# Kernel tuning notes

Measured on AMD Instinct MI355X. Metric: run time of the kernel, lower is better.

## Reference

```python
import jax, jax.numpy as jnp
import numpy as np

N_NODES = 50000
N_EDGES = 800000
G_DIM = 128
H1 = 32
HEADS = 4
H2 = 64
ATT_SLOPE = 0.2   # PyG GATConv default negative_slope
LRELU_SLOPE = 0.01  # F.leaky_relu default
BN_EPS = 1e-5


def segment_softmax(logits, seg, num_segments):
    # numerically stable softmax over edges grouped by destination node
    m = jax.ops.segment_max(logits, seg, num_segments=num_segments)
    e = jnp.exp(logits - m[seg])
    s = jax.ops.segment_sum(e, seg, num_segments=num_segments)
    return e / (s[seg] + 1e-16)


def gat_layer(x, src, dst, W, a_src, a_dst, bias, concat):
    # PyG GATConv: x' = W x ; alpha_e = softmax_dst(leaky_relu(a_src.x_src + a_dst.x_dst))
    N = x.shape[0]
    H, C = a_src.shape
    xw = (x @ W).reshape(N, H, C)          # [N,H,C]
    al_s = jnp.sum(xw * a_src, axis=-1)    # [N,H]
    al_d = jnp.sum(xw * a_dst, axis=-1)    # [N,H]
    logits = jax.nn.leaky_relu(al_s[src] + al_d[dst], ATT_SLOPE)  # [E,H]
    alpha = segment_softmax(logits, dst, N)                        # [E,H]
    out = jax.ops.segment_sum(alpha[:, :, None] * xw[src], dst, num_segments=N)  # [N,H,C]
    out = out.reshape(N, H * C) if concat else out.mean(axis=1)
    return out + bias


def batchnorm_train(x, gamma, beta):
    mu = x.mean(axis=0)
    var = x.var(axis=0)  # biased, as torch BN uses for normalization
    return (x - mu) * jax.lax.rsqrt(var + BN_EPS) * gamma + beta


def setup_inputs() -> dict:
    key = jax.random.key(0)
    ks = jax.random.split(key, 12)
    node_features = jax.random.normal(ks[0], (N_NODES, G_DIM), dtype=jnp.float32)
    node_type = jax.random.randint(ks[1], (N_NODES,), 0, 3)
    edge_index = jax.random.randint(ks[2], (2, N_EDGES), 0, N_NODES)
    s1 = 1.0 / np.sqrt(G_DIM)
    s2 = 1.0 / np.sqrt(H1 * HEADS)
    return {
        "node_features": node_features,
        "node_type": node_type,
        "edge_index": edge_index,
        "W1": jax.random.normal(ks[3], (G_DIM, HEADS * H1), dtype=jnp.float32) * s1,
        "a_src1": jax.random.normal(ks[4], (HEADS, H1), dtype=jnp.float32) * s1,
        "a_dst1": jax.random.normal(ks[5], (HEADS, H1), dtype=jnp.float32) * s1,
        "b1": jnp.zeros((HEADS * H1,), dtype=jnp.float32),
        "g1": jnp.ones((HEADS * H1,), dtype=jnp.float32),
        "beta1": jnp.zeros((HEADS * H1,), dtype=jnp.float32),
        "W2": jax.random.normal(ks[6], (HEADS * H1, H2), dtype=jnp.float32) * s2,
        "a_src2": jax.random.normal(ks[7], (1, H2), dtype=jnp.float32) * s2,
        "a_dst2": jax.random.normal(ks[8], (1, H2), dtype=jnp.float32) * s2,
        "b2": jnp.zeros((H2,), dtype=jnp.float32),
        "g2": jnp.ones((H2,), dtype=jnp.float32),
        "beta2": jnp.zeros((H2,), dtype=jnp.float32),
    }


def reference(node_features, node_type, edge_index, W1, a_src1, a_dst1, b1, g1, beta1,
              W2, a_src2, a_dst2, b2, g2, beta2):
    N = node_features.shape[0]
    loop = jnp.arange(N)
    src = jnp.concatenate([edge_index[0], loop])  # add_self_loops=True (PyG default)
    dst = jnp.concatenate([edge_index[1], loop])
    x = gat_layer(node_features, src, dst, W1, a_src1, a_dst1, b1, concat=True)
    x = jax.nn.leaky_relu(batchnorm_train(x, g1, beta1), LRELU_SLOPE)
    x = gat_layer(x, src, dst, W2, a_src2, a_dst2, b2, concat=False)
    x = jax.nn.leaky_relu(batchnorm_train(x, g2, beta2), LRELU_SLOPE)
    return x
```

## Files before the change

kernel.cpp:

```cpp
#include <hip/hip_runtime.h>
#include <hip/hip_fp16.h>

#define NN 50000
#define NE 800000
#define ET 850000
#define GD 128
#define D1 128
#define NH 4
#define D2 64
#define NB_SCAN 196
#define NBP 1024
#define NXCD 8
#define NPX 6250
#define NSB 32
#define ESL 26563
#define NHB 256
#define CAP 8192

typedef unsigned short u16;
typedef _Float16 half8_t __attribute__((ext_vector_type(8)));
typedef float    f32x4_t __attribute__((ext_vector_type(4)));

__device__ __forceinline__ float lrelu(float x, float s) { return x > 0.f ? x : s * x; }

__global__ void k_prepw(const float* __restrict__ W1, const float* __restrict__ W2,
                        __half* __restrict__ Wp1, __half* __restrict__ Wp2) {
    int idx = blockIdx.x * 256 + threadIdx.x;
    if (idx < 16384) {
        int i = idx & 7, l = (idx >> 3) & 63, nt = (idx >> 9) & 7, kk = idx >> 12;
        int k = kk * 32 + (l >> 4) * 8 + i, n = nt * 16 + (l & 15);
        Wp1[idx] = __float2half(W1[k * D1 + n]);
    } else if (idx < 24576) {
        int x2 = idx - 16384;
        int i = x2 & 7, l = (x2 >> 3) & 63, nt = (x2 >> 9) & 3, kk = x2 >> 11;
        int k = kk * 32 + (l >> 4) * 8 + i, n = nt * 16 + (l & 15);
        Wp2[x2] = __float2half(W2[k * D2 + n]);
    }
}

__global__ void k_histgemm1(const int* __restrict__ ei,
                            unsigned* __restrict__ ulist, u16* __restrict__ plist,
                            int* __restrict__ partial, int* __restrict__ mcount,
                            const float* __restrict__ x, const half8_t* __restrict__ wp,
                            const float* __restrict__ as, const float* __restrict__ ad,
                            __half* __restrict__ xw, float* __restrict__ al_s,
                            float* __restrict__ al_d) {
    __shared__ unsigned lh[NPX];
    __shared__ unsigned lk;
    if (blockIdx.x < NHB) {
        const int s = blockIdx.x & (NXCD - 1), j = blockIdx.x >> 3;
        const int lo = s * NPX;
        for (int i = threadIdx.x; i < NPX; i += 256) lh[i] = 0u;
        if (threadIdx.x == 0) lk = 0u;
        __syncthreads();
        const int e0 = j * ESL, e1 = min(ET, e0 + ESL);
        const size_t ub = (size_t)blockIdx.x * CAP;
        for (int e = e0 + threadIdx.x; e < e1; e += 256) {
            int d = (e < NE) ? ei[NE + e] : (e - NE);
            unsigned dl = (unsigned)(d - lo);
            if (dl < (unsigned)NPX) {
                unsigned p = atomicAdd(&lh[dl], 1u);
                int src = (e < NE) ? ei[e] : d;
                unsigned k = atomicAdd(&lk, 1u);
                ulist[ub + k] = (dl << 16) | (unsigned)src;
                plist[ub + k] = (u16)p;
            }
        }
        __syncthreads();
        const size_t pb = ((size_t)s * NSB + j) * NPX;
        for (int i = threadIdx.x; i < NPX; i += 256) partial[pb + i] = (int)lh[i];
        if (threadIdx.x == 0) mcount[blockIdx.x] = (int)lk;
        return;
    }
    const int strip = (blockIdx.x - NHB) * 4 + (threadIdx.x >> 6);
    if (strip >= NN / 16) return;
    const int l = threadIdx.x & 63;
    const int row0 = strip * 16;
    const int c = l & 15, g = l >> 4;
    const float* xrow = x + (size_t)(row0 + c) * GD;

    f32x4_t acc[8];
#pragma unroll
    for (int nt = 0; nt < 8; nt++) acc[nt] = (f32x4_t){0.f, 0.f, 0.f, 0.f};

#pragma unroll
    for (int kk = 0; kk < 4; kk++) {
        const int koff = kk * 32 + g * 8;
        f32x4_t a0 = *(const f32x4_t*)(xrow + koff);
        f32x4_t a1 = *(const f32x4_t*)(xrow + koff + 4);
        half8_t af;
#pragma unroll
        for (int i = 0; i < 4; i++) { af[i] = (_Float16)a0[i]; af[i + 4] = (_Float16)a1[i]; }
#pragma unroll
        for (int nt = 0; nt < 8; nt++) {
            half8_t bf = wp[(kk * 8 + nt) * 64 + l];
            acc[nt] = __builtin_amdgcn_mfma_f32_16x16x32_f16(af, bf, acc[nt], 0, 0, 0);
        }
    }

    float asv[8], adv[8];
#pragma unroll
    for (int nt = 0; nt < 8; nt++) { asv[nt] = as[nt * 16 + c]; adv[nt] = ad[nt * 16 + c]; }

#pragma unroll
    for (int r = 0; r < 4; r++) {
        const int row = row0 + g * 4 + r;
        __half* xwr = xw + (size_t)row * D1;
        float hs[4] = {0.f, 0.f, 0.f, 0.f}, hd[4] = {0.f, 0.f, 0.f, 0.f};
#pragma unroll
        for (int nt = 0; nt < 8; nt++) {
            float v = acc[nt][r];
            xwr[nt * 16 + c] = __float2half(v);
            hs[nt >> 1] += v * asv[nt];
            hd[nt >> 1] += v * adv[nt];
        }
#pragma unroll
        for (int m = 1; m <= 8; m <<= 1) {
#pragma unroll
            for (int h = 0; h < 4; h++) { hs[h] += __shfl_xor(hs[h], m); hd[h] += __shfl_xor(hd[h], m); }
        }
        if (c == 0) {
#pragma unroll
            for (int h = 0; h < 4; h++) { al_s[row * NH + h] = hs[h]; al_d[row * NH + h] = hd[h]; }
        }
    }
}

__global__ void k_nodeprefix(const int* __restrict__ partial, int* __restrict__ P,
                             int* __restrict__ cnt) {
    int d = blockIdx.x * 256 + threadIdx.x;
    if (d >= NN) return;
    int s = d / NPX, dl = d - s * NPX;
    size_t base = (size_t)s * NSB * NPX + dl;
    int run = 0;
    for (int j = 0; j < NSB; j++) {
        size_t idx = base + (size_t)j * NPX;
        P[idx] = run;
        run += partial[idx];
    }
    cnt[d] = run;
}

__global__ void k_blocksum(const int* __restrict__ cnt, int* __restrict__ part) {
    __shared__ int r[256];
    int t = threadIdx.x, i = blockIdx.x * 256 + t;
    r[t] = (i < NN) ? cnt[i] : 0;
    __syncthreads();
    for (int s = 128; s >= 1; s >>= 1) {
        if (t < s) r[t] += r[t + s];
        __syncthreads();
    }
    if (t == 0) part[blockIdx.x] = r[0];
}

__global__ void k_scanfix(const int* __restrict__ cnt, const int* __restrict__ part,
                          int* __restrict__ row_ptr) {
    __shared__ int pp[256];
    __shared__ int r[256];
    int b = blockIdx.x, t = threadIdx.x, i = b * 256 + t;
    pp[t] = (t < NB_SCAN) ? part[t] : 0;
    int v = (i < NN) ? cnt[i] : 0;
    r[t] = v;
    __syncthreads();
    for (int off = 1; off < 256; off <<= 1) {
        int pv = (t >= off) ? pp[t - off] : 0;
        int rv = (t >= off) ? r[t - off] : 0;
        __syncthreads();
        pp[t] += pv; r[t] += rv;
        __syncthreads();
    }
    int pbase = b ? pp[b - 1] : 0;
    if (i < NN) row_ptr[i] = pbase + (t ? r[t - 1] : 0);
    if (i == NN - 1) row_ptr[NN] = pbase + r[t];
}

__global__ void k_fill_x(const int* __restrict__ row_ptr, const int* __restrict__ P,
                         const unsigned* __restrict__ ulist, const u16* __restrict__ plist,
                         const int* __restrict__ mcount, u16* __restrict__ csr_src) {
    const int b = blockIdx.x;
    const int s = b & (NXCD - 1), j = b >> 3;
    const int lo = s * NPX;
    const int m = mcount[b];
    const size_t ub = (size_t)b * CAP;
    const size_t pb = ((size_t)s * NSB + j) * NPX;
    for (int k = threadIdx.x; k < m; k += 256) {
        unsigned u = ulist[ub + k];
        unsigned p = plist[ub + k];
        int dl = (int)(u >> 16);
        int base = row_ptr[lo + dl] + P[pb + dl];
        csr_src[base + p] = (u16)(u & 0xffffu);
    }
}

__global__ void k_gat1(const int* __restrict__ row_ptr, const u16* __restrict__ csr_src,
                       const float* __restrict__ als, const float* __restrict__ ald,
                       const __half2* __restrict__ xw, __half2* __restrict__ out) {
    const int b = blockIdx.x;
    const int d = (b & (NXCD - 1)) * NPX + (b >> 3);
    const int beg = row_ptr[d];
    const int deg = row_ptr[d + 1] - beg;
    const int lane = threadIdx.x;

    __shared__ int   s_src[64];
    __shared__ float s_al[64 * NH];

    const float4 adv = *(const float4*)(ald + d * NH);
    const int h = lane >> 4;

    float ax = 0.f, ay = 0.f, den = 0.f;
    for (int base = 0; base < deg; base += 64) {
        int cnt = min(64, deg - base);
        if (lane < cnt) {
            int s = csr_src[beg + base + lane];
            s_src[lane] = s;
            const float4 a = *(const float4*)(als + s * NH);
            s_al[lane * NH + 0] = __expf(lrelu(a.x + adv.x, 0.2f));
            s_al[lane * NH + 1] = __expf(lrelu(a.y + adv.y, 0.2f));
            s_al[lane * NH + 2] = __expf(lrelu(a.z + adv.z, 0.2f));
            s_al[lane * NH + 3] = __expf(lrelu(a.w + adv.w, 0.2f));
        }
        __syncthreads();
#pragma unroll 4
        for (int i = 0; i < cnt; i++) {
            float al = s_al[i * NH + h];
            float2 v = __half22float2(xw[(size_t)s_src[i] * 64 + lane]);
            den += al; ax += al * v.x; ay += al * v.y;
        }
        __syncthreads();
    }
    float inv = 1.f / (den + 1e-16f);
    __half2 hv;
    hv.x = __float2half(ax * inv);
    hv.y = __float2half(ay * inv);
    out[(size_t)d * 64 + lane] = hv;
}

__global__ void k_bnstats1h(const __half2* __restrict__ x, float* __restrict__ bp) {
    int t = threadIdx.x, bid = blockIdx.x;
    float s0 = 0.f, q0 = 0.f, s1 = 0.f, q1 = 0.f;
    for (int r = bid; r < NN; r += NBP) {
        float2 f = __half22float2(x[(size_t)r * 64 + t]);
        s0 += f.x; q0 += f.x * f.x;
        s1 += f.y; q1 += f.y * f.y;
    }
    bp[bid * D1 + 2 * t] = s0;
    bp[bid * D1 + 2 * t + 1] = s1;
    bp[NBP * D1 + bid * D1 + 2 * t] = q0;
    bp[NBP * D1 + bid * D1 + 2 * t + 1] = q1;
}

template <int D>
__global__ void k_bnstats(const float* __restrict__ x, float* __restrict__ bp) {
    int j = threadIdx.x, bid = blockIdx.x;
    float s = 0.f, q = 0.f;
    for (int r = bid; r < NN; r += NBP) {
        float v = x[(size_t)r * D + j];
        s += v; q += v * v;
    }
    bp[bid * D + j] = s;
    bp[NBP * D + bid * D + j] = q;
}

template <int D>
__global__ void k_bnreduce(const float* __restrict__ bp, const float* __restrict__ g,
                           const float* __restrict__ b, float* __restrict__ scale,
                           float* __restrict__ shift) {
    __shared__ float rs[256], rq[256];
    int j = blockIdx.x, t = threadIdx.x;
    float s = 0.f, q = 0.f;
    for (int i = t; i < NBP; i += 256) {
        s += bp[i * D + j];
        q += bp[NBP * D + i * D + j];
    }
    rs[t] = s; rq[t] = q;
    __syncthreads();
    for (int st = 128; st >= 1; st >>= 1) {
        if (t < st) { rs[t] += rs[t + st]; rq[t] += rq[t + st]; }
        __syncthreads();
    }
    if (t == 0) {
        float mu = rs[0] / (float)NN;
        float var = rq[0] / (float)NN - mu * mu;
        float sc = rsqrtf(var + 1e-5f) * g[j];
        scale[j] = sc;
        shift[j] = b[j] - mu * sc;
    }
}

__global__ void k_bnapply2(const float* __restrict__ x, const float* __restrict__ scale,
                           const float* __restrict__ shift, float* __restrict__ y) {
    int idx = blockIdx.x * blockDim.x + threadIdx.x;
    if (idx >= NN * D2 / 4) return;
    float4 v = ((const float4*)x)[idx];
    int c = (idx * 4) & (D2 - 1);
    v.x = lrelu(v.x * scale[c + 0] + shift[c + 0], 0.01f);
    v.y = lrelu(v.y * scale[c + 1] + shift[c + 1], 0.01f);
    v.z = lrelu(v.z * scale[c + 2] + shift[c + 2], 0.01f);
    v.w = lrelu(v.w * scale[c + 3] + shift[c + 3], 0.01f);
    ((float4*)y)[idx] = v;
}

__global__ void k_gemm2m(const __half* __restrict__ x, const float* __restrict__ scale,
                         const float* __restrict__ shift, const half8_t* __restrict__ wp,
                         const float* __restrict__ as, const float* __restrict__ ad,
                         __half* __restrict__ xw, float* __restrict__ al_s, float* __restrict__ al_d) {
    const int l = threadIdx.x;
    const int row0 = blockIdx.x * 16;
    const int c = l & 15, g = l >> 4;
    const __half* xrow = x + (size_t)(row0 + c) * D1;

    f32x4_t acc[4];
#pragma unroll
    for (int nt = 0; nt < 4; nt++) acc[nt] = (f32x4_t){0.f, 0.f, 0.f, 0.f};

#pragma unroll
    for (int kk = 0; kk < 4; kk++) {
        const int koff = kk * 32 + g * 8;
        half8_t a8 = *(const half8_t*)(xrow + koff);
        f32x4_t sc0 = *(const f32x4_t*)(scale + koff);
        f32x4_t sc1 = *(const f32x4_t*)(scale + koff + 4);
        f32x4_t sh0 = *(const f32x4_t*)(shift + koff);
        f32x4_t sh1 = *(const f32x4_t*)(shift + koff + 4);
        half8_t af;
#pragma unroll
        for (int i = 0; i < 4; i++) {
            af[i]     = (_Float16)lrelu((float)a8[i] * sc0[i] + sh0[i], 0.01f);
            af[i + 4] = (_Float16)lrelu((float)a8[i + 4] * sc1[i] + sh1[i], 0.01f);
        }
#pragma unroll
        for (int nt = 0; nt < 4; nt++) {
            half8_t bf = wp[(kk * 4 + nt) * 64 + l];
            acc[nt] = __builtin_amdgcn_mfma_f32_16x16x32_f16(af, bf, acc[nt], 0, 0, 0);
        }
    }

    float asv[4], adv[4];
#pragma unroll
    for (int nt = 0; nt < 4; nt++) { asv[nt] = as[nt * 16 + c]; adv[nt] = ad[nt * 16 + c]; }

#pragma unroll
    for (int r = 0; r < 4; r++) {
        const int row = row0 + g * 4 + r;
        __half* xwr = xw + (size_t)row * D2;
        float hs = 0.f, hd = 0.f;
#pragma unroll
        for (int nt = 0; nt < 4; nt++) {
            float v = acc[nt][r];
            xwr[nt * 16 + c] = __float2half(v);
            hs += v * asv[nt];
            hd += v * adv[nt];
        }
#pragma unroll
        for (int m = 1; m <= 8; m <<= 1) { hs += __shfl_xor(hs, m); hd += __shfl_xor(hd, m); }
        if (c == 0) { al_s[row] = hs; al_d[row] = hd; }
    }
}

__global__ void k_gat2(const int* __restrict__ row_ptr, const u16* __restrict__ csr_src,
                       const float* __restrict__ als, const float* __restrict__ ald,
                       const __half2* __restrict__ xw, float* __restrict__ out) {
    const int b = blockIdx.x;
    const int d = (b & (NXCD - 1)) * NPX + (b >> 3);
    const int beg = row_ptr[d];
    const int deg = row_ptr[d + 1] - beg;
    const int lane = threadIdx.x;
    const int sub = lane >> 5, l = lane & 31;

    const float add = ald[d];
    float ax = 0.f, ay = 0.f, den = 0.f;
    for (int base = 0; base < deg; base += 64) {
        int cnt = min(64, deg - base);
        int s = 0; float e = 0.f;
        if (lane < cnt) {
            s = csr_src[beg + base + lane];
            e = __expf(lrelu(als[s] + add, 0.2f));
        }
        int np = (cnt + 1) >> 1;
        for (int i = 0; i < np; i++) {
            int idx = 2 * i + sub;
            float al = __shfl(e, idx);
            int  si  = __shfl(s, idx);
            float2 v = __half22float2(xw[(size_t)si * 32 + l]);
            den += al; ax += al * v.x; ay += al * v.y;
        }
    }
    ax += __shfl_xor(ax, 32); ay += __shfl_xor(ay, 32); den += __shfl_xor(den, 32);
    if (lane < 32) {
        float inv = 1.f / (den + 1e-16f);
        *(float2*)(out + (size_t)d * D2 + 2 * l) = make_float2(ax * inv, ay * inv);
    }
}

extern "C" void kernel_launch(void* const* d_in, const int* in_sizes, int n_in,
                              void* d_out, int out_size, void* d_ws, size_t ws_size,
                              hipStream_t stream) {
    const float* x   = (const float*)d_in[0];
    const int*   ei  = (const int*)d_in[2];
    const float* W1  = (const float*)d_in[3];
    const float* as1 = (const float*)d_in[4];
    const float* ad1 = (const float*)d_in[5];
    const float* g1  = (const float*)d_in[7];
    const float* be1 = (const float*)d_in[8];
    const float* W2  = (const float*)d_in[9];
    const float* as2 = (const float*)d_in[10];
    const float* ad2 = (const float*)d_in[11];
    const float* g2  = (const float*)d_in[13];
    const float* be2 = (const float*)d_in[14];
    float* out = (float*)d_out;

    float* ws = (float*)d_ws;
    __half* xw1  = (__half*)ws;
    __half* xw2  = (__half*)ws;
    float* bp    = ws + 1600000;
    unsigned* ulist = (unsigned*)(ws + 3200000);
    u16*   plist  = (u16*)(ws + 5297152);
    int*   mcount = (int*)(ws + 6345728);
    int*   cnt    = (int*)(ws + 6345984);
    float* al_s2 = ws + 3200000;
    float* al_d2 = ws + 3250000;
    float* al_s1 = ws + 6400000;
    float* al_d1 = al_s1 + 200000;
    float* aggF  = al_d1 + 200000;
    __half* agg1 = (__half*)aggF;
    int*   partial = (int*)aggF;
    int*   Pbase   = (int*)(aggF + 1600000);
    int*   row_ptr = (int*)(aggF + 3200000);
    int*   part    = row_ptr + 50001;
    float* st      = (float*)(part + 249);
    u16*   csr_src = (u16*)(st + 768);
    __half* Wp1    = (__half*)(csr_src + 850000);
    __half* Wp2    = Wp1 + 16384;

    k_prepw<<<96, 256, 0, stream>>>(W1, W2, Wp1, Wp2);
    k_histgemm1<<<NHB + (NN / 16 + 3) / 4, 256, 0, stream>>>(
        ei, ulist, plist, partial, mcount, x, (const half8_t*)Wp1, as1, ad1, xw1, al_s1, al_d1);
    k_nodeprefix<<<NB_SCAN, 256, 0, stream>>>(partial, Pbase, cnt);
    k_blocksum<<<NB_SCAN, 256, 0, stream>>>(cnt, part);
    k_scanfix<<<NB_SCAN, 256, 0, stream>>>(cnt, part, row_ptr);
    k_fill_x<<<NHB, 256, 0, stream>>>(row_ptr, Pbase, ulist, plist, mcount, csr_src);

    k_gat1<<<NN, 64, 0, stream>>>(row_ptr, csr_src, al_s1, al_d1, (const __half2*)xw1,
                                  (__half2*)agg1);
    k_bnstats1h<<<NBP, 64, 0, stream>>>((const __half2*)agg1, bp);
    k_bnreduce<D1><<<D1, 256, 0, stream>>>(bp, g1, be1, st, st + 128);

    k_gemm2m<<<NN / 16, 64, 0, stream>>>(agg1, st, st + 128, (const half8_t*)Wp2, as2, ad2,
                                         xw2, al_s2, al_d2);
    k_gat2<<<NN, 64, 0, stream>>>(row_ptr, csr_src, al_s2, al_d2, (const __half2*)xw2, out);
    k_bnstats<D2><<<NBP, D2, 0, stream>>>(out, bp);
    k_bnreduce<D2><<<D2, 256, 0, stream>>>(bp, g2, be2, st + 256, st + 320);
    k_bnapply2<<<(NN * D2 / 4 + 255) / 256, 256, 0, stream>>>(out, st + 256, st + 320, out);
}
```

Before: 213.5 us.

## Split edge histogram into more blocks with packed u16 counters and separate self-loops

The histogram phase now runs across 1024 blocks over 128 edge slices instead of 256 blocks over 32. Per-node counters are packed two u16 per word in shared memory, and the per-slice partial counts are stored as u16, with the prefix written in place instead of into a separate int array. Self-loops are no longer fed through the histogram; they take slot 0 of each row (count +1) and are written by extra blocks in the fill kernel. This aims to cut shared-memory footprint and global traffic and to raise parallelism in the CSR build. It adds a CAP=1024 overflow guard that silently drops edges if a slice receives more than expected.

```diff
diff --git a/kernel.cpp b/kernel.cpp
--- a/kernel.cpp
+++ b/kernel.cpp
@@ -12,10 +12,10 @@
 #define NBP 1024
 #define NXCD 8
 #define NPX 6250
-#define NSB 32
-#define ESL 26563
-#define NHB 256
-#define CAP 8192
+#define HSL 128
+#define ESL 6250
+#define NHB 1024
+#define CAP 1024
 
 typedef unsigned short u16;
 typedef _Float16 half8_t __attribute__((ext_vector_type(8)));
@@ -40,35 +40,37 @@
 
 __global__ void k_histgemm1(const int* __restrict__ ei,
                             unsigned* __restrict__ ulist, u16* __restrict__ plist,
-                            int* __restrict__ partial, int* __restrict__ mcount,
+                            u16* __restrict__ partial, int* __restrict__ mcount,
                             const float* __restrict__ x, const half8_t* __restrict__ wp,
                             const float* __restrict__ as, const float* __restrict__ ad,
                             __half* __restrict__ xw, float* __restrict__ al_s,
                             float* __restrict__ al_d) {
-    __shared__ unsigned lh[NPX];
+    __shared__ unsigned lh[NPX / 2];
     __shared__ unsigned lk;
     if (blockIdx.x < NHB) {
         const int s = blockIdx.x & (NXCD - 1), j = blockIdx.x >> 3;
         const int lo = s * NPX;
-        for (int i = threadIdx.x; i < NPX; i += 256) lh[i] = 0u;
+        for (int i = threadIdx.x; i < NPX / 2; i += 256) lh[i] = 0u;
         if (threadIdx.x == 0) lk = 0u;
         __syncthreads();
-        const int e0 = j * ESL, e1 = min(ET, e0 + ESL);
+        const int e0 = j * ESL;
         const size_t ub = (size_t)blockIdx.x * CAP;
-        for (int e = e0 + threadIdx.x; e < e1; e += 256) {
-            int d = (e < NE) ? ei[NE + e] : (e - NE);
+        for (int e = e0 + threadIdx.x; e < e0 + ESL; e += 256) {
+            int d = ei[NE + e];
             unsigned dl = (unsigned)(d - lo);
             if (dl < (unsigned)NPX) {
-                unsigned p = atomicAdd(&lh[dl], 1u);
-                int src = (e < NE) ? ei[e] : d;
+                unsigned old = atomicAdd(&lh[dl >> 1], (dl & 1) ? 0x10000u : 1u);
+                unsigned p = (old >> ((dl & 1) * 16)) & 0xffffu;
                 unsigned k = atomicAdd(&lk, 1u);
-                ulist[ub + k] = (dl << 16) | (unsigned)src;
-                plist[ub + k] = (u16)p;
+                if (k < CAP) {
+                    ulist[ub + k] = (dl << 16) | (unsigned)ei[e];
+                    plist[ub + k] = (u16)p;
+                }
             }
         }
         __syncthreads();
-        const size_t pb = ((size_t)s * NSB + j) * NPX;
-        for (int i = threadIdx.x; i < NPX; i += 256) partial[pb + i] = (int)lh[i];
+        unsigned* pout = (unsigned*)(partial + (size_t)blockIdx.x * NPX);
+        for (int i = threadIdx.x; i < NPX / 2; i += 256) pout[i] = lh[i];
         if (threadIdx.x == 0) mcount[blockIdx.x] = (int)lk;
         return;
     }
@@ -126,19 +128,18 @@
     }
 }
 
-__global__ void k_nodeprefix(const int* __restrict__ partial, int* __restrict__ P,
-                             int* __restrict__ cnt) {
+__global__ void k_nodeprefix(u16* __restrict__ partial, int* __restrict__ cnt) {
     int d = blockIdx.x * 256 + threadIdx.x;
     if (d >= NN) return;
     int s = d / NPX, dl = d - s * NPX;
-    size_t base = (size_t)s * NSB * NPX + dl;
     int run = 0;
-    for (int j = 0; j < NSB; j++) {
-        size_t idx = base + (size_t)j * NPX;
-        P[idx] = run;
-        run += partial[idx];
-    }
-    cnt[d] = run;
+    for (int j = 0; j < HSL; j++) {
+        size_t idx = (size_t)(j * NXCD + s) * NPX + dl;
+        int v = partial[idx];
+        partial[idx] = (u16)run;
+        run += v;
+    }
+    cnt[d] = run + 1;
 }
 
 __global__ void k_blocksum(const int* __restrict__ cnt, int* __restrict__ part) {
@@ -174,21 +175,30 @@
     if (i == NN - 1) row_ptr[NN] = pbase + r[t];
 }
 
-__global__ void k_fill_x(const int* __restrict__ row_ptr, const int* __restrict__ P,
+__global__ void k_fill_x(const int* __restrict__ row_ptr, const u16* __restrict__ P,
                          const unsigned* __restrict__ ulist, const u16* __restrict__ plist,
                          const int* __restrict__ mcount, u16* __restrict__ csr_src) {
     const int b = blockIdx.x;
-    const int s = b & (NXCD - 1), j = b >> 3;
-    const int lo = s * NPX;
-    const int m = mcount[b];
-    const size_t ub = (size_t)b * CAP;
-    const size_t pb = ((size_t)s * NSB + j) * NPX;
-    for (int k = threadIdx.x; k < m; k += 256) {
-        unsigned u = ulist[ub + k];
-        unsigned p = plist[ub + k];
-        int dl = (int)(u >> 16);
-        int base = row_ptr[lo + dl] + P[pb + dl];
-        csr_src[base + p] = (u16)(u & 0xffffu);
+    if (b < NHB) {
+        const int s = b & (NXCD - 1);
+        const int lo = s * NPX;
+        const int m = min(mcount[b], CAP);
+        const size_t ub = (size_t)b * CAP;
+        const u16* Pb = P + (size_t)b * NPX;
+        for (int k = threadIdx.x; k < m; k += 256) {
+            unsigned u = ulist[ub + k];
+            int dl = (int)(u >> 16);
+            int base = row_ptr[lo + dl] + 1 + (int)Pb[dl] + (int)plist[ub + k];
+            csr_src[base] = (u16)(u & 0xffffu);
+        }
+        return;
+    }
+    const int b2 = b - NHB;
+    const int xcd = b2 & (NXCD - 1);
+    const int off = (b2 >> 3) * 256 + threadIdx.x;
+    if (off < NPX) {
+        int d = xcd * NPX + off;
+        csr_src[row_ptr[d]] = (u16)d;
     }
 }
 
@@ -413,17 +423,16 @@
     __half* xw2  = (__half*)ws;
     float* bp    = ws + 1600000;
     unsigned* ulist = (unsigned*)(ws + 3200000);
-    u16*   plist  = (u16*)(ws + 5297152);
-    int*   mcount = (int*)(ws + 6345728);
-    int*   cnt    = (int*)(ws + 6345984);
+    u16*   plist  = (u16*)(ws + 4248576);
+    int*   mcount = (int*)(ws + 4772864);
+    int*   cnt    = (int*)(ws + 4773888);
     float* al_s2 = ws + 3200000;
     float* al_d2 = ws + 3250000;
     float* al_s1 = ws + 6400000;
     float* al_d1 = al_s1 + 200000;
     float* aggF  = al_d1 + 200000;
     __half* agg1 = (__half*)aggF;
-    int*   partial = (int*)aggF;
-    int*   Pbase   = (int*)(aggF + 1600000);
+    u16*   partial = (u16*)aggF;
     int*   row_ptr = (int*)(aggF + 3200000);
     int*   part    = row_ptr + 50001;
     float* st      = (float*)(part + 249);
@@ -434,10 +443,10 @@
     k_prepw<<<96, 256, 0, stream>>>(W1, W2, Wp1, Wp2);
     k_histgemm1<<<NHB + (NN / 16 + 3) / 4, 256, 0, stream>>>(
         ei, ulist, plist, partial, mcount, x, (const half8_t*)Wp1, as1, ad1, xw1, al_s1, al_d1);
-    k_nodeprefix<<<NB_SCAN, 256, 0, stream>>>(partial, Pbase, cnt);
+    k_nodeprefix<<<NB_SCAN, 256, 0, stream>>>(partial, cnt);
     k_blocksum<<<NB_SCAN, 256, 0, stream>>>(cnt, part);
     k_scanfix<<<NB_SCAN, 256, 0, stream>>>(cnt, part, row_ptr);
-    k_fill_x<<<NHB, 256, 0, stream>>>(row_ptr, Pbase, ulist, plist, mcount, csr_src);
+    k_fill_x<<<NHB + 200, 256, 0, stream>>>(row_ptr, partial, ulist, plist, mcount, csr_src);
 
     k_gat1<<<NN, 64, 0, stream>>>(row_ptr, csr_src, al_s1, al_d1, (const __half2*)xw1,
                                   (__half2*)agg1);
```

Measured after the change: 182.2 us. 14.7% less time.
